# Kernel tuning notes

Measured on AMD Instinct MI355X. Metric: run time of the kernel, lower is better.

The kernel has to match this reference:

```python
import jax, jax.numpy as jnp
import numpy as np

N = 2097152   # number of points
TDIM = 16     # t_feat dim
HID = 64      # map_st hidden
BIG = 10000.0 # outer-bin extension from get_xy_compute


def setup_inputs() -> dict:
    key = jax.random.key(0)
    ks = jax.random.split(key, 4)
    x = jax.random.normal(ks[0], (N, 3), dtype=jnp.float32)
    t_feat = jax.random.normal(ks[1], (N, TDIM), dtype=jnp.float32)
    mask = jnp.array([1.0, 1.0, 0.0], dtype=jnp.float32)
    W1 = jax.random.normal(ks[2], (2 + TDIM, HID), dtype=jnp.float32) * 0.1
    b1 = jnp.zeros((HID,), dtype=jnp.float32)
    W2 = jax.random.normal(ks[3], (HID, 10), dtype=jnp.float32) * 0.1
    b2 = jnp.zeros((10,), dtype=jnp.float32)
    return {"x": x, "t_feat": t_feat, "mask": mask,
            "W1": W1, "b1": b1, "W2": W2, "b2": b2}


def _map_st(a, t, W1, b1, W2, b2):
    # a: [N,2] tanh of masked channels; t: [N,TDIM] -> [N,10] positive params
    z = jnp.concatenate([a, t], axis=-1)
    h = jax.nn.relu(z @ W1 + b1)
    return jax.nn.softplus(h @ W2 + b2) + 1e-4


def _get_xy(d):
    # d: [N,10] = dxl2,dxl1,dxr1,dxr2,dyl2,dyl1,dyr1,dyr2,kl,kr  (split order in get_all_xy)
    dxl2, dxl1, dxr1, dxr2 = d[..., 0], d[..., 1], d[..., 2], d[..., 3]
    dyl2, dyl1, dyr1, dyr2 = d[..., 4], d[..., 5], d[..., 6], d[..., 7]
    kl, kr = d[..., 8] * 2.0, d[..., 9] * 2.0
    xL1 = -dxl1;            yL1 = -dyl1
    xL2 = -dxl1 - dxl2;     yL2 = -dyl1 - dyl2
    xR1 = dxr1;             yR1 = dyr1
    xR2 = dxr1 + dxr2;      yR2 = dyr1 + dyr2
    xR3 = xR2 + BIG;        yR3 = yR2 + kr * BIG
    xL3 = xL2 - BIG;        yL3 = yL2 - kl * BIG
    all_x = jnp.stack([xL3, xL2, xL1, xR1, xR2, xR3], axis=-1)  # [N,6] monotonic
    all_y = jnp.stack([yL3, yL2, yL1, yR1, yR2, yR3], axis=-1)
    return all_x, all_y


def _interp(xk, yk, qx):
    # xk,yk: [N,6] knots; qx: [N]. Piecewise-linear interpolation (InterpGrad.forw_compute out).
    xl, xr = xk[..., :-1], xk[..., 1:]
    yl, yr = yk[..., :-1], yk[..., 1:]
    qx = jnp.clip(qx, xl[..., 0] * 0.99, xr[..., -1] * 0.99)
    q = qx[..., None]                       # [N,1]
    in_range = (q >= xl) & (q < xr)         # exactly one bin per row after clamp
    vals = (yr - yl) / (xr - xl) * (q - xl) + yl
    return jnp.sum(jnp.where(in_range, vals, 0.0), axis=-1)


def reference(x, t_feat, mask, W1, b1, W2, b2):
    # mask = [1,1,0]: channels 0,1 condition; channel 2 is transformed
    y_base = x * mask
    a = jnp.tanh(x[..., :2])
    d = _map_st(a, t_feat, W1, b1, W2, b2)
    all_x, all_y = _get_xy(d)
    out = _interp(all_x, all_y, x[..., 2])  # [N]
    return jnp.concatenate([y_base[..., :2], out[..., None]], axis=-1)
```

## Files before the change

### kernel.cpp

```cpp
#include <hip/hip_runtime.h>
#include <hip/hip_bf16.h>

typedef __attribute__((ext_vector_type(8))) short bf16x8;
typedef __attribute__((ext_vector_type(4))) float f32x4;
typedef __attribute__((ext_vector_type(4))) int   i32x4;

#define BIGC 10000.0f
#define TPW 2

__device__ __forceinline__ float fast_exp2(float x) { return __builtin_amdgcn_exp2f(x); }
__device__ __forceinline__ float fast_log2(float x) { return __builtin_amdgcn_logf(x); }
__device__ __forceinline__ float fast_rcp(float x)  { return __builtin_amdgcn_rcpf(x); }

__device__ __forceinline__ float fast_tanh(float x) {
    const float ax = fabsf(x);
    const float e  = fast_exp2(ax * 2.8853900817779268f);
    const float r  = 1.0f - 2.0f * fast_rcp(e + 1.0f);
    return copysignf(r, x);
}
__device__ __forceinline__ float fast_softplus_eps(float v) {
    const float e = fast_exp2(fabsf(v) * -1.4426950408889634f);
    const float l = fast_log2(1.0f + e) * 0.6931471805599453f;
    return fmaxf(v, 0.0f) + l + 0.0001f;
}
__device__ __forceinline__ unsigned pack2bf(float hi, float lo) {
    unsigned r;
    asm("v_cvt_pk_bf16_f32 %0, %1, %2" : "=v"(r) : "v"(lo), "v"(hi));
    return r;
}

__global__ void __launch_bounds__(64, 4) coupling_mfma8(
    const float* __restrict__ x, const float* __restrict__ t_feat,
    const float* __restrict__ mask, const float* __restrict__ W1,
    const float* __restrict__ b1, const float* __restrict__ W2,
    const float* __restrict__ b2, float* __restrict__ out, int n)
{
    __shared__ float lds_d[64][11];

    const int lane = threadIdx.x & 63;
    const int m    = lane & 15;
    const int q    = lane >> 4;
    const int m4   = m << 2;

    bf16x8 w1f[4];
#pragma unroll
    for (int a = 0; a < 4; ++a) {
        float wv[8];
#pragma unroll
        for (int j = 0; j < 8; ++j) {
            const int k = q * 8 + j;
            const int col = 16 * a + m;
            float v = 0.0f;
            if (k < 16)       v = W1[(k + 2) * 64 + col];
            else if (k == 16) v = W1[0 * 64 + col];
            else if (k == 17) v = W1[1 * 64 + col];
            else if (k == 18) v = b1[col];
            wv[j] = v;
        }
        i32x4 f = { (int)pack2bf(wv[1], wv[0]), (int)pack2bf(wv[3], wv[2]),
                    (int)pack2bf(wv[5], wv[4]), (int)pack2bf(wv[7], wv[6]) };
        w1f[a] = __builtin_bit_cast(bf16x8, f);
    }
    bf16x8 w2f[2];
#pragma unroll
    for (int fi = 0; fi < 2; ++fi) {
        float wv[8];
#pragma unroll
        for (int j = 0; j < 8; ++j) {
            const int hid = 32 * fi + 16 * (j >> 2) + 4 * q + (j & 3);
            wv[j] = (m < 10) ? W2[hid * 10 + m] : 0.0f;
        }
        i32x4 f = { (int)pack2bf(wv[1], wv[0]), (int)pack2bf(wv[3], wv[2]),
                    (int)pack2bf(wv[5], wv[4]), (int)pack2bf(wv[7], wv[6]) };
        w2f[fi] = __builtin_bit_cast(bf16x8, f);
    }
    const float bias2 = (m < 10) ? b2[m] : 0.0f;
    const float m0 = mask[0], m1 = mask[1];

    for (int it = 0; it < TPW; ++it) {
        int pb = (blockIdx.x * TPW + it) * 64;
        pb = max(min(pb, n - 64), 0);

        const int pl = pb + lane;
        const float* xp = x + pl * 3;
        const float xi0 = xp[0], xi1 = xp[1], xi2 = xp[2];

        float4 ta[4], tb[4];
        if (q < 2) {
#pragma unroll
            for (int s = 0; s < 4; ++s) {
                const float4* tr = (const float4*)(t_feat + (pb + 16 * s + m) * 16 + q * 8);
                ta[s] = tr[0];
                tb[s] = tr[1];
            }
        }

        const unsigned pk = pack2bf(fast_tanh(xi1), fast_tanh(xi0));

#pragma unroll
        for (int s = 0; s < 4; ++s) {
            const int tp = __builtin_amdgcn_ds_bpermute(s * 64 + m4, (int)pk);

            i32x4 zw = { 0, 0, 0, 0 };
            if (q < 2) {
                zw[0] = (int)pack2bf(ta[s].y, ta[s].x);
                zw[1] = (int)pack2bf(ta[s].w, ta[s].z);
                zw[2] = (int)pack2bf(tb[s].y, tb[s].x);
                zw[3] = (int)pack2bf(tb[s].w, tb[s].z);
            } else if (q == 2) {
                zw[0] = tp;
                zw[1] = 0x3F80;
            }
            const bf16x8 zf = __builtin_bit_cast(bf16x8, zw);

            f32x4 acc[4];
#pragma unroll
            for (int a = 0; a < 4; ++a) {
                f32x4 c = { 0.0f, 0.0f, 0.0f, 0.0f };
                acc[a] = __builtin_amdgcn_mfma_f32_16x16x32_bf16(w1f[a], zf, c, 0, 0, 0);
            }

            float rl[16];
#pragma unroll
            for (int a = 0; a < 4; ++a)
#pragma unroll
                for (int r = 0; r < 4; ++r)
                    rl[4 * a + r] = fmaxf(acc[a][r], 0.0f);
            i32x4 a20 = { (int)pack2bf(rl[1],  rl[0]),  (int)pack2bf(rl[3],  rl[2]),
                          (int)pack2bf(rl[5],  rl[4]),  (int)pack2bf(rl[7],  rl[6]) };
            i32x4 a21 = { (int)pack2bf(rl[9],  rl[8]),  (int)pack2bf(rl[11], rl[10]),
                          (int)pack2bf(rl[13], rl[12]), (int)pack2bf(rl[15], rl[14]) };

            f32x4 cb = { bias2, bias2, bias2, bias2 };
            f32x4 cz = { 0.0f, 0.0f, 0.0f, 0.0f };
            f32x4 cd0 = __builtin_amdgcn_mfma_f32_16x16x32_bf16(
                            __builtin_bit_cast(bf16x8, a20), w2f[0], cb, 0, 0, 0);
            f32x4 cd1 = __builtin_amdgcn_mfma_f32_16x16x32_bf16(
                            __builtin_bit_cast(bf16x8, a21), w2f[1], cz, 0, 0, 0);

#pragma unroll
            for (int r = 0; r < 4; ++r) {
                const float dv = cd0[r] + cd1[r];
                if (m < 10) lds_d[16 * s + 4 * q + r][m] = dv;
            }
        }

        {
            const float* dd = lds_d[lane];
            const float dxl2 = fast_softplus_eps(dd[0]);
            const float dxl1 = fast_softplus_eps(dd[1]);
            const float dxr1 = fast_softplus_eps(dd[2]);
            const float dxr2 = fast_softplus_eps(dd[3]);
            const float dyl2 = fast_softplus_eps(dd[4]);
            const float dyl1 = fast_softplus_eps(dd[5]);
            const float dyr1 = fast_softplus_eps(dd[6]);
            const float dyr2 = fast_softplus_eps(dd[7]);
            const float kl = fast_softplus_eps(dd[8]) * 2.0f;
            const float kr = fast_softplus_eps(dd[9]) * 2.0f;

            const float xL1 = -dxl1,        yL1 = -dyl1;
            const float xL2 = -dxl1 - dxl2, yL2 = -dyl1 - dyl2;
            const float xR1 = dxr1,         yR1 = dyr1;
            const float xR2 = dxr1 + dxr2,  yR2 = dyr1 + dyr2;
            const float xR3 = xR2 + BIGC,   yR3 = fmaf(kr, BIGC, yR2);
            const float xL3 = xL2 - BIGC,   yL3 = fmaf(-kl, BIGC, yL2);

            float qx = fminf(fmaxf(xi2, xL3 * 0.99f), xR3 * 0.99f);
            float xl = xL3, xrr = xL2, yl = yL3, yr = yL2;
            if (qx >= xL2) { xl = xL2; xrr = xL1; yl = yL2; yr = yL1; }
            if (qx >= xL1) { xl = xL1; xrr = xR1; yl = yL1; yr = yR1; }
            if (qx >= xR1) { xl = xR1; xrr = xR2; yl = yR1; yr = yR2; }
            if (qx >= xR2) { xl = xR2; xrr = xR3; yl = yR2; yr = yR3; }
            const float slope = (yr - yl) * fast_rcp(xrr - xl);
            const float res = fmaf(slope, qx - xl, yl);

            float* op = out + pl * 3;
            op[0] = xi0 * m0;
            op[1] = xi1 * m1;
            op[2] = res;
        }
    }
}

extern "C" void kernel_launch(void* const* d_in, const int* in_sizes, int n_in,
                              void* d_out, int out_size, void* d_ws, size_t ws_size,
                              hipStream_t stream) {
    const float* x      = (const float*)d_in[0];
    const float* t_feat = (const float*)d_in[1];
    const float* mask   = (const float*)d_in[2];
    const float* W1     = (const float*)d_in[3];
    const float* b1     = (const float*)d_in[4];
    const float* W2     = (const float*)d_in[5];
    const float* b2     = (const float*)d_in[6];
    float* out = (float*)d_out;

    const int n = in_sizes[0] / 3;
    const int pts_per_block = TPW * 64;
    const int grid = (n + pts_per_block - 1) / pts_per_block;
    coupling_mfma8<<<grid, 64, 0, stream>>>(x, t_feat, mask, W1, b1, W2, b2, out, n);
}
```

Baseline: 236.0 us.

## Split fused kernel into MFMA MLP pass and separate interpolation pass via workspace

Splits the single fused kernel in two. The first runs the bf16 MFMA MLP and writes the 10 pre-softplus parameters per point to a column-major workspace buffer. The second, launched with 256 threads, applies softplus and the piecewise interpolation. This drops the LDS staging and the per-lane serial epilogue in the narrow 64-thread kernel, and it lifts occupancy for the MLP kernel, at the cost of an extra 80 MB of global round-trip traffic and a second launch. The fused path remains as a fallback when no workspace is provided.

```diff
diff --git a/kernel.cpp b/kernel.cpp
--- a/kernel.cpp
+++ b/kernel.cpp
@@ -27,6 +27,164 @@
     unsigned r;
     asm("v_cvt_pk_bf16_f32 %0, %1, %2" : "=v"(r) : "v"(lo), "v"(hi));
     return r;
+}
+
+
+__global__ void __launch_bounds__(64, 6) coupling_mlp(
+    const float* __restrict__ x, const float* __restrict__ t_feat,
+    const float* __restrict__ W1, const float* __restrict__ b1,
+    const float* __restrict__ W2, const float* __restrict__ b2,
+    float* __restrict__ dws, int n)
+{
+    const int lane = threadIdx.x & 63;
+    const int m    = lane & 15;
+    const int q    = lane >> 4;
+    const int m4   = m << 2;
+
+    bf16x8 w1f[4];
+#pragma unroll
+    for (int a = 0; a < 4; ++a) {
+        float wv[8];
+#pragma unroll
+        for (int j = 0; j < 8; ++j) {
+            const int k = q * 8 + j;
+            const int col = 16 * a + m;
+            float v = 0.0f;
+            if (k < 16)       v = W1[(k + 2) * 64 + col];
+            else if (k == 16) v = W1[0 * 64 + col];
+            else if (k == 17) v = W1[1 * 64 + col];
+            else if (k == 18) v = b1[col];
+            wv[j] = v;
+        }
+        i32x4 f = { (int)pack2bf(wv[1], wv[0]), (int)pack2bf(wv[3], wv[2]),
+                    (int)pack2bf(wv[5], wv[4]), (int)pack2bf(wv[7], wv[6]) };
+        w1f[a] = __builtin_bit_cast(bf16x8, f);
+    }
+    bf16x8 w2f[2];
+#pragma unroll
+    for (int fi = 0; fi < 2; ++fi) {
+        float wv[8];
+#pragma unroll
+        for (int j = 0; j < 8; ++j) {
+            const int hid = 32 * fi + 16 * (j >> 2) + 4 * q + (j & 3);
+            wv[j] = (m < 10) ? W2[hid * 10 + m] : 0.0f;
+        }
+        i32x4 f = { (int)pack2bf(wv[1], wv[0]), (int)pack2bf(wv[3], wv[2]),
+                    (int)pack2bf(wv[5], wv[4]), (int)pack2bf(wv[7], wv[6]) };
+        w2f[fi] = __builtin_bit_cast(bf16x8, f);
+    }
+    const float bias2 = (m < 10) ? b2[m] : 0.0f;
+
+    for (int it = 0; it < TPW; ++it) {
+        int pb = (blockIdx.x * TPW + it) * 64;
+        pb = max(min(pb, n - 64), 0);
+
+        const float* xp = x + (pb + lane) * 3;
+        const float xi0 = xp[0], xi1 = xp[1];
+
+        float4 ta[4], tb[4];
+        if (q < 2) {
+#pragma unroll
+            for (int s = 0; s < 4; ++s) {
+                const float4* tr = (const float4*)(t_feat + (pb + 16 * s + m) * 16 + q * 8);
+                ta[s] = tr[0];
+                tb[s] = tr[1];
+            }
+        }
+
+        const unsigned pk = pack2bf(fast_tanh(xi1), fast_tanh(xi0));
+
+#pragma unroll
+        for (int s = 0; s < 4; ++s) {
+            const int tp = __builtin_amdgcn_ds_bpermute(s * 64 + m4, (int)pk);
+
+            i32x4 zw = { 0, 0, 0, 0 };
+            if (q < 2) {
+                zw[0] = (int)pack2bf(ta[s].y, ta[s].x);
+                zw[1] = (int)pack2bf(ta[s].w, ta[s].z);
+                zw[2] = (int)pack2bf(tb[s].y, tb[s].x);
+                zw[3] = (int)pack2bf(tb[s].w, tb[s].z);
+            } else if (q == 2) {
+                zw[0] = tp;
+                zw[1] = 0x3F80;
+            }
+            const bf16x8 zf = __builtin_bit_cast(bf16x8, zw);
+
+            f32x4 acc[4];
+#pragma unroll
+            for (int a = 0; a < 4; ++a) {
+                f32x4 c = { 0.0f, 0.0f, 0.0f, 0.0f };
+                acc[a] = __builtin_amdgcn_mfma_f32_16x16x32_bf16(w1f[a], zf, c, 0, 0, 0);
+            }
+
+            float rl[16];
+#pragma unroll
+            for (int a = 0; a < 4; ++a)
+#pragma unroll
+                for (int r = 0; r < 4; ++r)
+                    rl[4 * a + r] = fmaxf(acc[a][r], 0.0f);
+            i32x4 a20 = { (int)pack2bf(rl[1],  rl[0]),  (int)pack2bf(rl[3],  rl[2]),
+                          (int)pack2bf(rl[5],  rl[4]),  (int)pack2bf(rl[7],  rl[6]) };
+            i32x4 a21 = { (int)pack2bf(rl[9],  rl[8]),  (int)pack2bf(rl[11], rl[10]),
+                          (int)pack2bf(rl[13], rl[12]), (int)pack2bf(rl[15], rl[14]) };
+
+            f32x4 cb = { bias2, bias2, bias2, bias2 };
+            f32x4 cz = { 0.0f, 0.0f, 0.0f, 0.0f };
+            f32x4 cd0 = __builtin_amdgcn_mfma_f32_16x16x32_bf16(
+                            __builtin_bit_cast(bf16x8, a20), w2f[0], cb, 0, 0, 0);
+            f32x4 cd1 = __builtin_amdgcn_mfma_f32_16x16x32_bf16(
+                            __builtin_bit_cast(bf16x8, a21), w2f[1], cz, 0, 0, 0);
+
+            if (m < 10) {
+                f32x4 dsum = { cd0[0] + cd1[0], cd0[1] + cd1[1],
+                               cd0[2] + cd1[2], cd0[3] + cd1[3] };
+                float4* dst = (float4*)(dws + (size_t)m * n + pb + 16 * s + 4 * q);
+                *dst = make_float4(dsum[0], dsum[1], dsum[2], dsum[3]);
+            }
+        }
+    }
+}
+
+__global__ void __launch_bounds__(256, 8) coupling_interp(
+    const float* __restrict__ x, const float* __restrict__ mask,
+    const float* __restrict__ dws, float* __restrict__ out, int n)
+{
+    const int p = blockIdx.x * 256 + threadIdx.x;
+    if (p >= n) return;
+
+    const float m0 = mask[0], m1 = mask[1];
+    const float* xp = x + (size_t)p * 3;
+    const float xi0 = xp[0], xi1 = xp[1], xi2 = xp[2];
+
+    float dv[10];
+#pragma unroll
+    for (int f = 0; f < 10; ++f)
+        dv[f] = fast_softplus_eps(dws[(size_t)f * n + p]);
+
+    const float dxl2 = dv[0], dxl1 = dv[1], dxr1 = dv[2], dxr2 = dv[3];
+    const float dyl2 = dv[4], dyl1 = dv[5], dyr1 = dv[6], dyr2 = dv[7];
+    const float kl = dv[8] * 2.0f, kr = dv[9] * 2.0f;
+
+    const float xL1 = -dxl1,        yL1 = -dyl1;
+    const float xL2 = -dxl1 - dxl2, yL2 = -dyl1 - dyl2;
+    const float xR1 = dxr1,         yR1 = dyr1;
+    const float xR2 = dxr1 + dxr2,  yR2 = dyr1 + dyr2;
+    const float xR3 = xR2 + BIGC,   yR3 = fmaf(kr, BIGC, yR2);
+    const float xL3 = xL2 - BIGC,   yL3 = fmaf(-kl, BIGC, yL2);
+
+    float qx = fminf(fmaxf(xi2, xL3 * 0.99f), xR3 * 0.99f);
+    float xl = xL3, xrr = xL2, yl = yL3, yr = yL2;
+    if (qx >= xL2) { xl = xL2; xrr = xL1; yl = yL2; yr = yL1; }
+    if (qx >= xL1) { xl = xL1; xrr = xR1; yl = yL1; yr = yR1; }
+    if (qx >= xR1) { xl = xR1; xrr = xR2; yl = yR1; yr = yR2; }
+    if (qx >= xR2) { xl = xR2; xrr = xR3; yl = yR2; yr = yR3; }
+    const float slope = (yr - yl) * fast_rcp(xrr - xl);
+    const float res = fmaf(slope, qx - xl, yl);
+
+    float* op = out + (size_t)p * 3;
+    op[0] = xi0 * m0;
+    op[1] = xi1 * m1;
+    op[2] = res;
 }
 
 __global__ void __launch_bounds__(64, 4) coupling_mfma8(
@@ -195,7 +353,18 @@
     float* out = (float*)d_out;
 
     const int n = in_sizes[0] / 3;
-    const int pts_per_block = TPW * 64;
-    const int grid = (n + pts_per_block - 1) / pts_per_block;
-    coupling_mfma8<<<grid, 64, 0, stream>>>(x, t_feat, mask, W1, b1, W2, b2, out, n);
-}
+    const size_t need = (size_t)10 * (size_t)n * sizeof(float);
+
+    if (d_ws != nullptr && ws_size >= need) {
+        float* dws = (float*)d_ws;
+        const int ppb_a = TPW * 64;
+        const int grid_a = (n + ppb_a - 1) / ppb_a;
+        coupling_mlp<<<grid_a, 64, 0, stream>>>(x, t_feat, W1, b1, W2, b2, dws, n);
+        const int grid_b = (n + 255) / 256;
+        coupling_interp<<<grid_b, 256, 0, stream>>>(x, mask, dws, out, n);
+    } else {
+        const int pts_per_block = TPW * 64;
+        const int grid = (n + pts_per_block - 1) / pts_per_block;
+        coupling_mfma8<<<grid, 64, 0, stream>>>(x, t_feat, mask, W1, b1, W2, b2, out, n);
+    }
+}
```

Result: slower. 305.3 us (+29.4%).
